# Optimization experiments

Measured on AMD Instinct MI355X. Metric: run time of the kernel, lower is better.

Reference implementation:

```python
import jax, jax.numpy as jnp
import numpy as np

FEATURE_DIM = 512
ACTION_DIM = 32
N_EXPERTS = 4
D_HIDDEN = 256
BATCH = 131072


def setup_inputs() -> dict:
    key = jax.random.key(0)
    ks = jax.random.split(key, 7)
    s_in = 1.0 / np.sqrt(FEATURE_DIM)
    s_h = 1.0 / np.sqrt(D_HIDDEN)
    return {
        "features": jax.random.normal(ks[0], (BATCH, FEATURE_DIM), dtype=jnp.float32),
        # gating network: feature_dim -> n_experts
        "Wg": jax.random.normal(ks[1], (FEATURE_DIM, N_EXPERTS), dtype=jnp.float32) * s_in,
        "bg": jnp.zeros((N_EXPERTS,), dtype=jnp.float32),
        # per-expert 2-layer MLP: feature_dim -> d_hidden -> action_dim
        "W1": jax.random.normal(ks[2], (N_EXPERTS, FEATURE_DIM, D_HIDDEN), dtype=jnp.float32) * s_in,
        "b1": jnp.zeros((N_EXPERTS, D_HIDDEN), dtype=jnp.float32),
        "W2": jax.random.normal(ks[3], (N_EXPERTS, D_HIDDEN, ACTION_DIM), dtype=jnp.float32) * s_h,
        "b2": jnp.zeros((N_EXPERTS, ACTION_DIM), dtype=jnp.float32),
    }


def reference(features, Wg, bg, W1, b1, W2, b2):
    # gate: softmax over experts, shape [b, e]
    gate = jax.nn.softmax(features @ Wg + bg, axis=-1)
    # expert MLPs (dense MoE: every expert sees every token)
    h = jax.nn.relu(jnp.einsum("bf,efh->beh", features, W1) + b1)  # [b, e, h]
    expert_out = jnp.einsum("beh,eha->bea", h, W2) + b2            # [b, e, a]
    # gate-weighted mixture -> action mean [b, a]
    action_mean = jnp.einsum("bea,be->ba", expert_out, gate)
    return action_mean
```

## Files before the change

### kernel.cpp

```cpp
#include <hip/hip_runtime.h>
#include <hip/hip_bf16.h>
#include <math.h>

#define FDIM 512
#define NEXP 4
#define HDIM 256
#define ADIM 32
#define BM   64
#define NTHR 512

typedef __attribute__((ext_vector_type(8))) short frag8;
typedef __attribute__((ext_vector_type(4))) float f32x4;

#define W1T_OFF 0
#define W2T_OFF (4*256*512)
#define WGT_OFF (W2T_OFF + 4*32*256)

__device__ inline ushort f2bf(float x) {
    union { float f; unsigned u; } v; v.f = x;
    unsigned r = v.u + 0x7FFFu + ((v.u >> 16) & 1u);
    return (ushort)(r >> 16);
}

__device__ inline frag8 pack8(f32x4 a, f32x4 b) {
    frag8 r;
    r[0] = (short)f2bf(a[0]); r[1] = (short)f2bf(a[1]);
    r[2] = (short)f2bf(a[2]); r[3] = (short)f2bf(a[3]);
    r[4] = (short)f2bf(b[0]); r[5] = (short)f2bf(b[1]);
    r[6] = (short)f2bf(b[2]); r[7] = (short)f2bf(b[3]);
    return r;
}

__global__ __launch_bounds__(256) void moe_prep(const float* __restrict__ Wg,
                                                const float* __restrict__ W1,
                                                const float* __restrict__ W2,
                                                ushort* __restrict__ ws) {
    const int b = blockIdx.x, t = threadIdx.x;
    if (b < 64) {
        #pragma unroll
        for (int it = 0; it < 4; ++it) {
            int oct = (b * 256 + t) + it * 16384;
            int n = oct & 255, k8 = (oct >> 8) & 63, e = oct >> 14;
            f32x4 v0, v1;
            #pragma unroll
            for (int j = 0; j < 4; ++j) v0[j] = W1[(e*512 + k8*8 + j)*256 + n];
            #pragma unroll
            for (int j = 0; j < 4; ++j) v1[j] = W1[(e*512 + k8*8 + 4 + j)*256 + n];
            *(frag8*)(ws + W1T_OFF + (e*HDIM + n)*FDIM + k8*8) = pack8(v0, v1);
        }
    } else if (b < 80) {
        int oct = (b - 64) * 256 + t;
        int a = oct & 31, n8 = (oct >> 5) & 31, e = oct >> 10;
        f32x4 v0, v1;
        #pragma unroll
        for (int j = 0; j < 4; ++j) v0[j] = W2[(e*HDIM + n8*8 + j)*ADIM + a];
        #pragma unroll
        for (int j = 0; j < 4; ++j) v1[j] = W2[(e*HDIM + n8*8 + 4 + j)*ADIM + a];
        *(frag8*)(ws + W2T_OFF + (e*ADIM + a)*HDIM + n8*8) = pack8(v0, v1);
    } else {
        int oct = (b - 80) * 256 + t;
        int k8 = oct & 63, c = oct >> 6;
        f32x4 v0 = {0,0,0,0}, v1 = {0,0,0,0};
        if (c < NEXP) {
            #pragma unroll
            for (int j = 0; j < 4; ++j) v0[j] = Wg[(k8*8 + j)*NEXP + c];
            #pragma unroll
            for (int j = 0; j < 4; ++j) v1[j] = Wg[(k8*8 + 4 + j)*NEXP + c];
        }
        *(frag8*)(ws + WGT_OFF + c*FDIM + k8*8) = pack8(v0, v1);
    }
}

__global__ __launch_bounds__(NTHR, 2) void moe_main(
        const float* __restrict__ feat, const float* __restrict__ bg,
        const float* __restrict__ b1,  const float* __restrict__ b2,
        const ushort* __restrict__ ws, float* __restrict__ out) {
    __shared__ __attribute__((aligned(16))) unsigned char smem[65536 + 65536 + 1024];
    unsigned char* fbuf = smem;
    unsigned char* hbuf = smem + 65536;
    float* gate = (float*)(smem + 131072);

    const int tid = threadIdx.x;
    const int lane = tid & 63;
    const int wave = tid >> 6;
    const int l15 = lane & 15;
    const int lg  = lane >> 4;
    const int row0 = blockIdx.x * BM;
    const ushort* w1t = ws + W1T_OFF;
    const ushort* w2t = ws + W2T_OFF;
    const ushort* wgt = ws + WGT_OFF;

    {
        const float* fsrc = feat + (size_t)row0 * FDIM;
        #pragma unroll
        for (int it = 0; it < 8; ++it) {
            int c = tid + it * NTHR;
            int r = c >> 6, c8 = c & 63;
            const float* p = fsrc + r * FDIM + c8 * 8;
            f32x4 v0 = *(const f32x4*)p;
            f32x4 v1 = *(const f32x4*)(p + 4);
            *(frag8*)(fbuf + r * 1024 + ((c8 * 16) ^ ((r & 7) << 4))) = pack8(v0, v1);
        }
    }
    __syncthreads();

    if (wave < 4) {
        const int rt = wave;
        const int arow = rt * 16 + l15;
        const int aswz = (arow & 7) << 4;
        f32x4 acc = {0.f, 0.f, 0.f, 0.f};
        #pragma unroll
        for (int s = 0; s < 16; ++s) {
            int k8 = s * 4 + lg;
            frag8 a = *(const frag8*)(fbuf + arow * 1024 + ((k8 * 16) ^ aswz));
            frag8 bb = *(const frag8*)(wgt + l15 * FDIM + k8 * 8);
            acc = __builtin_amdgcn_mfma_f32_16x16x32_bf16(a, bb, acc, 0, 0, 0);
        }
        if (l15 < NEXP) {
            float bgv = bg[l15];
            #pragma unroll
            for (int r = 0; r < 4; ++r)
                gate[(rt * 16 + lg * 4 + r) * 4 + l15] = acc[r] + bgv;
        }
    }
    __syncthreads();
    if (tid < BM) {
        f32x4 g = *(const f32x4*)(gate + tid * 4);
        float m = fmaxf(fmaxf(g[0], g[1]), fmaxf(g[2], g[3]));
        float e0 = expf(g[0]-m), e1 = expf(g[1]-m), e2 = expf(g[2]-m), e3 = expf(g[3]-m);
        float inv = 1.f / (e0 + e1 + e2 + e3);
        f32x4 r = { e0*inv, e1*inv, e2*inv, e3*inv };
        *(f32x4*)(gate + tid * 4) = r;
    }
    __syncthreads();

    const int rt2 = wave >> 1, ct2 = wave & 1;
    f32x4 gv[4];
    #pragma unroll
    for (int r = 0; r < 4; ++r)
        gv[r] = *(const f32x4*)(gate + (rt2 * 16 + lg * 4 + r) * 4);
    f32x4 act = {0.f, 0.f, 0.f, 0.f};

    #pragma unroll
    for (int p = 0; p < 2; ++p) {
        f32x4 acc[2][4][2];
        #pragma unroll
        for (int eo = 0; eo < 2; ++eo)
            #pragma unroll
            for (int rt = 0; rt < 4; ++rt)
                #pragma unroll
                for (int ct = 0; ct < 2; ++ct)
                    acc[eo][rt][ct] = (f32x4){0.f, 0.f, 0.f, 0.f};

        #pragma unroll 4
        for (int s = 0; s < 16; ++s) {
            int k8 = s * 4 + lg;
            frag8 a[4];
            #pragma unroll
            for (int rt = 0; rt < 4; ++rt) {
                int arow = rt * 16 + l15;
                a[rt] = *(const frag8*)(fbuf + arow * 1024 + ((k8 * 16) ^ ((arow & 7) << 4)));
            }
            frag8 bb[2][2];
            #pragma unroll
            for (int eo = 0; eo < 2; ++eo)
                #pragma unroll
                for (int ct = 0; ct < 2; ++ct) {
                    int col = (wave * 2 + ct) * 16 + l15;
                    bb[eo][ct] = *(const frag8*)(w1t + ((2*p + eo) * HDIM + col) * FDIM + k8 * 8);
                }
            #pragma unroll
            for (int eo = 0; eo < 2; ++eo)
                #pragma unroll
                for (int rt = 0; rt < 4; ++rt)
                    #pragma unroll
                    for (int ct = 0; ct < 2; ++ct)
                        acc[eo][rt][ct] = __builtin_amdgcn_mfma_f32_16x16x32_bf16(
                            a[rt], bb[eo][ct], acc[eo][rt][ct], 0, 0, 0);
        }

        __syncthreads();
        #pragma unroll
        for (int eo = 0; eo < 2; ++eo) {
            int e = 2 * p + eo;
            #pragma unroll
            for (int ct = 0; ct < 2; ++ct) {
                int col = (wave * 2 + ct) * 16 + l15;
                float bias = b1[e * HDIM + col];
                #pragma unroll
                for (int rt = 0; rt < 4; ++rt)
                    #pragma unroll
                    for (int r = 0; r < 4; ++r) {
                        int row = rt * 16 + lg * 4 + r;
                        float v = fmaxf(acc[eo][rt][ct][r] + bias, 0.f);
                        *(ushort*)(hbuf + eo * 32768 + row * 512 +
                                   ((2 * col) ^ ((row & 7) << 4))) = f2bf(v);
                    }
            }
        }
        __syncthreads();

        #pragma unroll
        for (int eo = 0; eo < 2; ++eo) {
            int e = 2 * p + eo;
            const int arow = rt2 * 16 + l15;
            const int aswz = (arow & 7) << 4;
            const unsigned char* hb = hbuf + eo * 32768;
            f32x4 o = {0.f, 0.f, 0.f, 0.f};
            #pragma unroll
            for (int s = 0; s < 8; ++s) {
                int k8 = s * 4 + lg;
                frag8 a = *(const frag8*)(hb + arow * 512 + ((k8 * 16) ^ aswz));
                frag8 bb = *(const frag8*)(w2t + (e * ADIM + ct2 * 16 + l15) * HDIM + k8 * 8);
                o = __builtin_amdgcn_mfma_f32_16x16x32_bf16(a, bb, o, 0, 0, 0);
            }
            #pragma unroll
            for (int r = 0; r < 4; ++r)
                act[r] += gv[r][2*p + eo] * o[r];
        }
    }

    {
        int col = ct2 * 16 + l15;
        float b2v0 = b2[0*ADIM + col], b2v1 = b2[1*ADIM + col];
        float b2v2 = b2[2*ADIM + col], b2v3 = b2[3*ADIM + col];
        #pragma unroll
        for (int r = 0; r < 4; ++r) {
            int row = row0 + rt2 * 16 + lg * 4 + r;
            float bs = gv[r][0]*b2v0 + gv[r][1]*b2v1 + gv[r][2]*b2v2 + gv[r][3]*b2v3;
            out[(size_t)row * ADIM + col] = act[r] + bs;
        }
    }
}

extern "C" void kernel_launch(void* const* d_in, const int* in_sizes, int n_in,
                              void* d_out, int out_size, void* d_ws, size_t ws_size,
                              hipStream_t stream) {
    const float* feat = (const float*)d_in[0];
    const float* Wg   = (const float*)d_in[1];
    const float* bg   = (const float*)d_in[2];
    const float* W1   = (const float*)d_in[3];
    const float* b1   = (const float*)d_in[4];
    const float* W2   = (const float*)d_in[5];
    const float* b2   = (const float*)d_in[6];
    float* out = (float*)d_out;
    ushort* ws = (ushort*)d_ws;

    moe_prep<<<84, 256, 0, stream>>>(Wg, W1, W2, ws);
    const int nblk = (131072 + BM - 1) / BM;
    moe_main<<<nblk, NTHR, 0, stream>>>(feat, bg, b1, b2, ws, out);
}
```

Measured before the change: 679.3 us.

## Restructure MoE kernel: register-resident features, LDS-staged W1 via async global loads

```diff
diff --git a/kernel.cpp b/kernel.cpp
--- a/kernel.cpp
+++ b/kernel.cpp
@@ -6,7 +6,7 @@
 #define NEXP 4
 #define HDIM 256
 #define ADIM 32
-#define BM   64
+#define BM   128
 #define NTHR 512
 
 typedef __attribute__((ext_vector_type(8))) short frag8;
@@ -31,6 +31,12 @@
     return r;
 }
 
+__device__ __forceinline__ void gl16(const void* g, void* l) {
+    __builtin_amdgcn_global_load_lds(
+        (const __attribute__((address_space(1))) unsigned int*)g,
+        (__attribute__((address_space(3))) unsigned int*)l, 16, 0, 0);
+}
+
 __global__ __launch_bounds__(256) void moe_prep(const float* __restrict__ Wg,
                                                 const float* __restrict__ W1,
                                                 const float* __restrict__ W2,
@@ -75,10 +81,11 @@
         const float* __restrict__ feat, const float* __restrict__ bg,
         const float* __restrict__ b1,  const float* __restrict__ b2,
         const ushort* __restrict__ ws, float* __restrict__ out) {
-    __shared__ __attribute__((aligned(16))) unsigned char smem[65536 + 65536 + 1024];
-    unsigned char* fbuf = smem;
-    unsigned char* hbuf = smem + 65536;
-    float* gate = (float*)(smem + 131072);
+    __shared__ __attribute__((aligned(16))) unsigned char smem[65536 + 65536 + 16384 + 2048];
+    unsigned char* bufA = smem;
+    unsigned char* bufB = smem + 65536;
+    unsigned char* wgtb = smem + 131072;
+    float*         wgate = (float*)(smem + 147456);
 
     const int tid = threadIdx.x;
     const int lane = tid & 63;
@@ -86,151 +93,157 @@
     const int l15 = lane & 15;
     const int lg  = lane >> 4;
     const int row0 = blockIdx.x * BM;
-    const ushort* w1t = ws + W1T_OFF;
+    const int wrow = row0 + wave * 16;
     const ushort* w2t = ws + W2T_OFF;
-    const ushort* wgt = ws + WGT_OFF;
+    const char* w1b = (const char*)(ws + W1T_OFF);
+    const char* wgb = (const char*)(ws + WGT_OFF);
+
+    int sOff[8];
+    #pragma unroll
+    for (int j = 0; j < 8; ++j) {
+        int slot = j * 512 + tid;
+        int col  = slot >> 4;
+        int kkp  = ((slot & 15) * 16) ^ ((col & 7) << 4);
+        sOff[j]  = col * 1024 + kkp;
+    }
+    int gOff[2];
+    #pragma unroll
+    for (int j = 0; j < 2; ++j) {
+        int slot = j * 512 + tid;
+        int col  = slot >> 6;
+        int off  = (slot & 63) * 16;
+        gOff[j]  = col * 1024 + (off ^ ((col & 7) << 4));
+    }
+
+    #pragma unroll
+    for (int j = 0; j < 2; ++j)
+        gl16(wgb + gOff[j], wgtb + j * 8192 + wave * 1024);
+    #pragma unroll
+    for (int j = 0; j < 8; ++j)
+        gl16(w1b + sOff[j], bufA + j * 8192 + wave * 1024);
+
+    frag8 afrag[16];
+    const float* fp = feat + (size_t)(wrow + l15) * FDIM + lg * 8;
+    #pragma unroll
+    for (int g4 = 0; g4 < 4; ++g4) {
+        f32x4 t0[4], t1[4];
+        #pragma unroll
+        for (int s = 0; s < 4; ++s) {
+            const float* p = fp + (g4 * 4 + s) * 32;
+            t0[s] = *(const f32x4*)p;
+            t1[s] = *(const f32x4*)(p + 4);
+        }
+        #pragma unroll
+        for (int s = 0; s < 4; ++s) afrag[g4 * 4 + s] = pack8(t0[s], t1[s]);
+    }
+
+    __syncthreads();
 
     {
-        const float* fsrc = feat + (size_t)row0 * FDIM;
-        #pragma unroll
-        for (int it = 0; it < 8; ++it) {
-            int c = tid + it * NTHR;
-            int r = c >> 6, c8 = c & 63;
-            const float* p = fsrc + r * FDIM + c8 * 8;
-            f32x4 v0 = *(const f32x4*)p;
-            f32x4 v1 = *(const f32x4*)(p + 4);
-            *(frag8*)(fbuf + r * 1024 + ((c8 * 16) ^ ((r & 7) << 4))) = pack8(v0, v1);
-        }
-    }
-    __syncthreads();
-
-    if (wave < 4) {
-        const int rt = wave;
-        const int arow = rt * 16 + l15;
-        const int aswz = (arow & 7) << 4;
-        f32x4 acc = {0.f, 0.f, 0.f, 0.f};
+        f32x4 ga = {0.f, 0.f, 0.f, 0.f};
         #pragma unroll
         for (int s = 0; s < 16; ++s) {
-            int k8 = s * 4 + lg;
-            frag8 a = *(const frag8*)(fbuf + arow * 1024 + ((k8 * 16) ^ aswz));
-            frag8 bb = *(const frag8*)(wgt + l15 * FDIM + k8 * 8);
-            acc = __builtin_amdgcn_mfma_f32_16x16x32_bf16(a, bb, acc, 0, 0, 0);
-        }
-        if (l15 < NEXP) {
-            float bgv = bg[l15];
-            #pragma unroll
-            for (int r = 0; r < 4; ++r)
-                gate[(rt * 16 + lg * 4 + r) * 4 + l15] = acc[r] + bgv;
-        }
-    }
-    __syncthreads();
-    if (tid < BM) {
-        f32x4 g = *(const f32x4*)(gate + tid * 4);
-        float m = fmaxf(fmaxf(g[0], g[1]), fmaxf(g[2], g[3]));
-        float e0 = expf(g[0]-m), e1 = expf(g[1]-m), e2 = expf(g[2]-m), e3 = expf(g[3]-m);
-        float inv = 1.f / (e0 + e1 + e2 + e3);
-        f32x4 r = { e0*inv, e1*inv, e2*inv, e3*inv };
-        *(f32x4*)(gate + tid * 4) = r;
-    }
-    __syncthreads();
-
-    const int rt2 = wave >> 1, ct2 = wave & 1;
-    f32x4 gv[4];
-    #pragma unroll
-    for (int r = 0; r < 4; ++r)
-        gv[r] = *(const f32x4*)(gate + (rt2 * 16 + lg * 4 + r) * 4);
-    f32x4 act = {0.f, 0.f, 0.f, 0.f};
-
-    #pragma unroll
-    for (int p = 0; p < 2; ++p) {
-        f32x4 acc[2][4][2];
-        #pragma unroll
-        for (int eo = 0; eo < 2; ++eo)
-            #pragma unroll
-            for (int rt = 0; rt < 4; ++rt)
+            frag8 bb = *(const frag8*)(wgtb + l15 * 1024 + ((s * 64 + lg * 16) ^ ((l15 & 7) << 4)));
+            ga = __builtin_amdgcn_mfma_f32_16x16x32_bf16(afrag[s], bb, ga, 0, 0, 0);
+        }
+        float bgv = bg[l15 & 3];
+        #pragma unroll
+        for (int r = 0; r < 4; ++r) {
+            float v = ga[r] + bgv;
+            float m = fmaxf(v, __shfl_xor(v, 1));
+            m = fmaxf(m, __shfl_xor(m, 2));
+            float eV = expf(v - m);
+            float sV = eV + __shfl_xor(eV, 1);
+            sV += __shfl_xor(sV, 2);
+            float g = eV / sV;
+            if (l15 < NEXP) wgate[wave * 64 + (lg * 4 + r) * 4 + l15] = g;
+        }
+    }
+
+    f32x4 act[2];
+    act[0] = (f32x4){0.f, 0.f, 0.f, 0.f};
+    act[1] = (f32x4){0.f, 0.f, 0.f, 0.f};
+
+    for (int e = 0; e < NEXP; ++e) {
+        f32x4 acc1[16];
+        #pragma unroll
+        for (int ct = 0; ct < 16; ++ct) acc1[ct] = (f32x4){0.f, 0.f, 0.f, 0.f};
+
+        const char* wbase = w1b + e * 262144;
+
+        #pragma unroll
+        for (int c = 0; c < 4; ++c) {
+            if (c < 3) {
+                unsigned char* dst = ((c + 1) & 1) ? bufB : bufA;
                 #pragma unroll
-                for (int ct = 0; ct < 2; ++ct)
-                    acc[eo][rt][ct] = (f32x4){0.f, 0.f, 0.f, 0.f};
-
-        #pragma unroll 4
-        for (int s = 0; s < 16; ++s) {
-            int k8 = s * 4 + lg;
-            frag8 a[4];
-            #pragma unroll
-            for (int rt = 0; rt < 4; ++rt) {
-                int arow = rt * 16 + l15;
-                a[rt] = *(const frag8*)(fbuf + arow * 1024 + ((k8 * 16) ^ ((arow & 7) << 4)));
-            }
-            frag8 bb[2][2];
-            #pragma unroll
-            for (int eo = 0; eo < 2; ++eo)
+                for (int j = 0; j < 8; ++j)
+                    gl16(wbase + (c + 1) * 256 + sOff[j], dst + j * 8192 + wave * 1024);
+            }
+            __syncthreads();
+            unsigned char* src = (c & 1) ? bufB : bufA;
+            #pragma unroll
+            for (int s = 0; s < 4; ++s) {
                 #pragma unroll
-                for (int ct = 0; ct < 2; ++ct) {
-                    int col = (wave * 2 + ct) * 16 + l15;
-                    bb[eo][ct] = *(const frag8*)(w1t + ((2*p + eo) * HDIM + col) * FDIM + k8 * 8);
+                for (int ct = 0; ct < 16; ++ct) {
+                    frag8 bb = *(const frag8*)(src + (ct * 16 + l15) * 256 +
+                                               ((s * 64 + lg * 16) ^ ((l15 & 7) << 4)));
+                    acc1[ct] = __builtin_amdgcn_mfma_f32_16x16x32_bf16(
+                        afrag[c * 4 + s], bb, acc1[ct], 0, 0, 0);
                 }
-            #pragma unroll
-            for (int eo = 0; eo < 2; ++eo)
-                #pragma unroll
-                for (int rt = 0; rt < 4; ++rt)
-                    #pragma unroll
-                    for (int ct = 0; ct < 2; ++ct)
-                        acc[eo][rt][ct] = __builtin_amdgcn_mfma_f32_16x16x32_bf16(
-                            a[rt], bb[eo][ct], acc[eo][rt][ct], 0, 0, 0);
-        }
-
-        __syncthreads();
-        #pragma unroll
-        for (int eo = 0; eo < 2; ++eo) {
-            int e = 2 * p + eo;
-            #pragma unroll
-            for (int ct = 0; ct < 2; ++ct) {
-                int col = (wave * 2 + ct) * 16 + l15;
-                float bias = b1[e * HDIM + col];
-                #pragma unroll
-                for (int rt = 0; rt < 4; ++rt)
-                    #pragma unroll
-                    for (int r = 0; r < 4; ++r) {
-                        int row = rt * 16 + lg * 4 + r;
-                        float v = fmaxf(acc[eo][rt][ct][r] + bias, 0.f);
-                        *(ushort*)(hbuf + eo * 32768 + row * 512 +
-                                   ((2 * col) ^ ((row & 7) << 4))) = f2bf(v);
-                    }
-            }
-        }
-        __syncthreads();
-
-        #pragma unroll
-        for (int eo = 0; eo < 2; ++eo) {
-            int e = 2 * p + eo;
-            const int arow = rt2 * 16 + l15;
-            const int aswz = (arow & 7) << 4;
-            const unsigned char* hb = hbuf + eo * 32768;
-            f32x4 o = {0.f, 0.f, 0.f, 0.f};
-            #pragma unroll
-            for (int s = 0; s < 8; ++s) {
-                int k8 = s * 4 + lg;
-                frag8 a = *(const frag8*)(hb + arow * 512 + ((k8 * 16) ^ aswz));
-                frag8 bb = *(const frag8*)(w2t + (e * ADIM + ct2 * 16 + l15) * HDIM + k8 * 8);
-                o = __builtin_amdgcn_mfma_f32_16x16x32_bf16(a, bb, o, 0, 0, 0);
-            }
-            #pragma unroll
-            for (int r = 0; r < 4; ++r)
-                act[r] += gv[r][2*p + eo] * o[r];
-        }
-    }
-
-    {
-        int col = ct2 * 16 + l15;
-        float b2v0 = b2[0*ADIM + col], b2v1 = b2[1*ADIM + col];
-        float b2v2 = b2[2*ADIM + col], b2v3 = b2[3*ADIM + col];
-        #pragma unroll
-        for (int r = 0; r < 4; ++r) {
-            int row = row0 + rt2 * 16 + lg * 4 + r;
-            float bs = gv[r][0]*b2v0 + gv[r][1]*b2v1 + gv[r][2]*b2v2 + gv[r][3]*b2v3;
-            out[(size_t)row * ADIM + col] = act[r] + bs;
-        }
-    }
+            }
+            if (c < 3) __syncthreads();
+        }
+
+        unsigned char* hb = bufA + wave * 8192;
+        #pragma unroll
+        for (int ct = 0; ct < 16; ++ct) {
+            float b1v = b1[e * HDIM + ct * 16 + l15];
+            #pragma unroll
+            for (int r = 0; r < 4; ++r) {
+                int row = lg * 4 + r;
+                float v = fmaxf(acc1[ct][r] + b1v, 0.f);
+                *(ushort*)(hb + row * 512 + (((ct * 16 + l15) * 2) ^ ((row & 7) << 4))) = f2bf(v);
+            }
+        }
+        asm volatile("s_waitcnt lgkmcnt(0)" ::: "memory");
+        __builtin_amdgcn_sched_barrier(0);
+
+        f32x4 acc2[2];
+        acc2[0] = (f32x4){0.f, 0.f, 0.f, 0.f};
+        acc2[1] = (f32x4){0.f, 0.f, 0.f, 0.f};
+        #pragma unroll
+        for (int s2 = 0; s2 < 8; ++s2) {
+            frag8 ha = *(const frag8*)(hb + l15 * 512 + ((s2 * 64 + lg * 16) ^ ((l15 & 7) << 4)));
+            #pragma unroll
+            for (int ct2 = 0; ct2 < 2; ++ct2) {
+                frag8 bb = *(const frag8*)(w2t + (e * ADIM + ct2 * 16 + l15) * HDIM + (s2 * 4 + lg) * 8);
+                acc2[ct2] = __builtin_amdgcn_mfma_f32_16x16x32_bf16(ha, bb, acc2[ct2], 0, 0, 0);
+            }
+        }
+        #pragma unroll
+        for (int ct2 = 0; ct2 < 2; ++ct2) {
+            float b2v = b2[e * ADIM + ct2 * 16 + l15];
+            #pragma unroll
+            for (int r = 0; r < 4; ++r) {
+                float g = wgate[wave * 64 + (lg * 4 + r) * 4 + e];
+                act[ct2][r] += g * (acc2[ct2][r] + b2v);
+            }
+        }
+
+        if (e < 3) {
+            __syncthreads();
+            const char* nb = w1b + (e + 1) * 262144;
+            #pragma unroll
+            for (int j = 0; j < 8; ++j)
+                gl16(nb + sOff[j], bufA + j * 8192 + wave * 1024);
+        }
+    }
+
+    #pragma unroll
+    for (int ct2 = 0; ct2 < 2; ++ct2)
+        #pragma unroll
+        for (int r = 0; r < 4; ++r)
+            out[(size_t)(wrow + lg * 4 + r) * ADIM + ct2 * 16 + l15] = act[ct2][r];
 }
 
 extern "C" void kernel_launch(void* const* d_in, const int* in_sizes, int n_in,
@@ -247,6 +260,6 @@
     ushort* ws = (ushort*)d_ws;
 
     moe_prep<<<84, 256, 0, stream>>>(Wg, W1, W2, ws);
-    const int nblk = (131072 + BM - 1) / BM;
+    const int nblk = 131072 / BM;
     moe_main<<<nblk, NTHR, 0, stream>>>(feat, bg, b1, b2, ws, out);
 }
```

Result: slower. 694.6 us (+2.3%).
